# Performance work log

Measured on AMD Instinct MI355X. Metric: run time of the kernel, lower is better.

## Reference

```python
import jax, jax.numpy as jnp
import numpy as np

INV_SQRT2 = 0.7071067811865476
SCALES = 3


def dwt_analysis(x, dec_lo, dec_hi, scales):
    """Multi-level 1D DWT along last axis (pywt/ptwt convention).
    x: [B, D]. dec_lo/dec_hi are cross-correlation filters (torch conv1d
    semantics, i.e. the flipped pywt decomposition filters as stored by the
    repo). Returns [cA_s | cD_s | ... | cD_1] truncated to the last D columns
    (identity for Haar on power-of-two D)."""
    flen = dec_lo.shape[0]
    pad = (2 * flen - 3) // 2  # ptwt zero-pad; 0 for Haar (flen=2)
    filt = jnp.stack([dec_lo, dec_hi])[:, None, :]  # [2, 1, flen]
    lo = x[:, None, :]  # [B, 1, D]
    highs = []
    for _ in range(scales):
        out = jax.lax.conv_general_dilated(
            lo, filt, window_strides=(2,), padding=[(pad, pad)],
            dimension_numbers=('NCH', 'OIH', 'NCH'))  # [B, 2, D/2]
        lo = out[:, 0:1, :]
        highs.append(out[:, 1, :])
    coeffs = jnp.concatenate([lo[:, 0, :]] + highs[::-1], axis=-1)
    return coeffs[:, -x.shape[-1]:]


def setup_inputs() -> dict:
    key = jax.random.key(0)
    k1, k2, k3, k4, k5 = jax.random.split(key, 5)
    B, D = 4096, 4096
    x = jax.random.normal(k1, (B, D), jnp.float32)
    diag_s = jax.random.normal(k2, (D,), jnp.float32)
    diag_g = jax.random.normal(k3, (D,), jnp.float32)
    diag_b = jax.random.normal(k4, (D,), jnp.float32)
    perm = jax.random.permutation(k5, jnp.arange(D))  # random column permutation
    # Haar analysis filters in cross-correlation (torch conv1d) orientation
    dec_lo = jnp.array([INV_SQRT2, INV_SQRT2], jnp.float32)
    dec_hi = jnp.array([INV_SQRT2, -INV_SQRT2], jnp.float32)
    return {"x": x, "diag_s": diag_s, "diag_g": diag_g, "diag_b": diag_b,
            "dec_lo": dec_lo, "dec_hi": dec_hi, "perm": perm, "scales": SCALES}


def reference(x, diag_s, diag_g, diag_b, dec_lo, dec_hi, perm, scales):
    # mul_b: x @ diag(b) == columnwise scale (same math, no O(d^2) matmul)
    h = x * diag_b
    h = dwt_analysis(h, dec_lo, dec_hi, scales)
    # mul_p: x @ P for a permutation matrix == column gather
    h = jnp.take(h, perm, axis=1)
    h = h * diag_g  # mul_g
    h = dwt_analysis(h, dec_lo, dec_hi, scales)
    return h * diag_s  # mul_s
```

## Files before the change

kernel.cpp:

```cpp
#include <hip/hip_runtime.h>


#define D   4096
#define NT  256
#define R   4

#define C_INV_SQRT2 0.70710678118654752440f

typedef float vf2 __attribute__((ext_vector_type(2)));
typedef float vf4 __attribute__((ext_vector_type(4)));

static __device__ __forceinline__ int swz(int i) {
    return i ^ ((i >> 5) & 31);
}

static __device__ __forceinline__ void dwt3_reg(const float v[16],
                                                float a3[2], float d3[2],
                                                float d2[4], float d1[8]) {
    float a1[8];
    #pragma unroll
    for (int j = 0; j < 8; ++j) {
        a1[j] = (v[2 * j] + v[2 * j + 1]) * C_INV_SQRT2;
        d1[j] = (v[2 * j] - v[2 * j + 1]) * C_INV_SQRT2;
    }
    float a2[4];
    #pragma unroll
    for (int j = 0; j < 4; ++j) {
        a2[j] = (a1[2 * j] + a1[2 * j + 1]) * C_INV_SQRT2;
        d2[j] = (a1[2 * j] - a1[2 * j + 1]) * C_INV_SQRT2;
    }
    #pragma unroll
    for (int j = 0; j < 2; ++j) {
        a3[j] = (a2[2 * j] + a2[2 * j + 1]) * C_INV_SQRT2;
        d3[j] = (a2[2 * j] - a2[2 * j + 1]) * C_INV_SQRT2;
    }
}

__global__ __launch_bounds__(NT) void wavelet_rows_kernel(
    const float* __restrict__ x,
    const float* __restrict__ diag_s,
    const float* __restrict__ diag_g,
    const float* __restrict__ diag_b,
    const int*   __restrict__ perm,
    float*       __restrict__ out)
{
    __shared__ float buf[2][D];

    const int t = threadIdx.x;
    const size_t row0 = (size_t)blockIdx.x * R;

    float db[16], dg[16];
    int   pidx[16];
    {
        const vf4* b4 = (const vf4*)diag_b;
        const vf4* g4 = (const vf4*)diag_g;
        const int4* p4 = (const int4*)perm;
        #pragma unroll
        for (int k = 0; k < 4; ++k) {
            vf4 bv = b4[4 * t + k];
            db[4 * k + 0] = bv.x; db[4 * k + 1] = bv.y;
            db[4 * k + 2] = bv.z; db[4 * k + 3] = bv.w;
            vf4 gv = g4[4 * t + k];
            dg[4 * k + 0] = gv.x; dg[4 * k + 1] = gv.y;
            dg[4 * k + 2] = gv.z; dg[4 * k + 3] = gv.w;
            int4 pv = p4[4 * t + k];
            pidx[4 * k + 0] = pv.x; pidx[4 * k + 1] = pv.y;
            pidx[4 * k + 2] = pv.z; pidx[4 * k + 3] = pv.w;
        }
    }
    vf2 sA, sD3;
    vf4 sD2, sD1a, sD1b;
    {
        const vf2* s2 = (const vf2*)diag_s;
        const vf4* s4 = (const vf4*)diag_s;
        sA   = s2[t];
        sD3  = s2[256 + t];
        sD2  = s4[256 + t];
        sD1a = s4[512 + 2 * t];
        sD1b = s4[512 + 2 * t + 1];
    }

    for (int r = 0; r < R; ++r) {
        float* b = buf[r & 1];
        const vf4* x4 = (const vf4*)(x + (row0 + r) * (size_t)D);

        float v[16];
        #pragma unroll
        for (int k = 0; k < 4; ++k) {
            vf4 xv = x4[4 * t + k];
            v[4 * k + 0] = xv.x * db[4 * k + 0];
            v[4 * k + 1] = xv.y * db[4 * k + 1];
            v[4 * k + 2] = xv.z * db[4 * k + 2];
            v[4 * k + 3] = xv.w * db[4 * k + 3];
        }

        float a3[2], d3[2], d2[4], d1[8];
        dwt3_reg(v, a3, d3, d2, d1);

        #pragma unroll
        for (int j = 0; j < 2; ++j) b[swz(2 * t + j)]        = a3[j];
        #pragma unroll
        for (int j = 0; j < 2; ++j) b[swz(512 + 2 * t + j)]  = d3[j];
        #pragma unroll
        for (int j = 0; j < 4; ++j) b[swz(1024 + 4 * t + j)] = d2[j];
        #pragma unroll
        for (int j = 0; j < 8; ++j) b[swz(2048 + 8 * t + j)] = d1[j];

        __syncthreads();

        float w[16];
        #pragma unroll
        for (int k = 0; k < 16; ++k) {
            w[k] = b[swz(pidx[k])] * dg[k];
        }

        float b3[2], e3[2], e2[4], e1[8];
        dwt3_reg(w, b3, e3, e2, e1);

        float* orow = out + (row0 + r) * (size_t)D;
        {
            vf2* o2 = (vf2*)orow;
            vf2 ov;
            ov.x = b3[0] * sA.x;  ov.y = b3[1] * sA.y;
            __builtin_nontemporal_store(ov, &o2[t]);
            ov.x = e3[0] * sD3.x; ov.y = e3[1] * sD3.y;
            __builtin_nontemporal_store(ov, &o2[256 + t]);

            vf4* o4 = (vf4*)orow;
            vf4 o;
            o.x = e2[0] * sD2.x; o.y = e2[1] * sD2.y;
            o.z = e2[2] * sD2.z; o.w = e2[3] * sD2.w;
            __builtin_nontemporal_store(o, &o4[256 + t]);
            o.x = e1[0] * sD1a.x; o.y = e1[1] * sD1a.y;
            o.z = e1[2] * sD1a.z; o.w = e1[3] * sD1a.w;
            __builtin_nontemporal_store(o, &o4[512 + 2 * t]);
            o.x = e1[4] * sD1b.x; o.y = e1[5] * sD1b.y;
            o.z = e1[6] * sD1b.z; o.w = e1[7] * sD1b.w;
            __builtin_nontemporal_store(o, &o4[512 + 2 * t + 1]);
        }
    }
}

extern "C" void kernel_launch(void* const* d_in, const int* in_sizes, int n_in,
                              void* d_out, int out_size, void* d_ws, size_t ws_size,
                              hipStream_t stream) {
    const float* x      = (const float*)d_in[0];
    const float* diag_s = (const float*)d_in[1];
    const float* diag_g = (const float*)d_in[2];
    const float* diag_b = (const float*)d_in[3];
    const int* perm     = (const int*)d_in[6];
    float* out          = (float*)d_out;

    const int B = 4096 / R;
    wavelet_rows_kernel<<<B, NT, 0, stream>>>(x, diag_s, diag_g, diag_b, perm, out);
}
```

Before: 128.7 us.

## Prefetch next row into registers and use lightweight LDS-only barrier

Software-pipelines the row loop: the next row of x is loaded into registers before the current row's DWT and LDS exchange, so global-load latency overlaps with compute. The loop is fully unrolled and the __syncthreads is replaced with an LDS-only wait plus s_barrier, which does not wait on outstanding global loads. Launch bounds now request 4 blocks per CU. The cost is extra registers for the prefetched row, which may pressure occupancy.

After: 149.3 us. +16.0%, slower.

```diff
diff --git a/kernel.cpp b/kernel.cpp
--- a/kernel.cpp
+++ b/kernel.cpp
@@ -12,6 +12,13 @@
 
 static __device__ __forceinline__ int swz(int i) {
     return i ^ ((i >> 5) & 31);
+}
+
+static __device__ __forceinline__ void lds_barrier() {
+    __builtin_amdgcn_sched_barrier(0);
+    asm volatile("s_waitcnt lgkmcnt(0)" ::: "memory");
+    __builtin_amdgcn_s_barrier();
+    __builtin_amdgcn_sched_barrier(0);
 }
 
 static __device__ __forceinline__ void dwt3_reg(const float v[16],
@@ -36,7 +43,7 @@
     }
 }
 
-__global__ __launch_bounds__(NT) void wavelet_rows_kernel(
+__global__ __launch_bounds__(NT, 4) void wavelet_rows_kernel(
     const float* __restrict__ x,
     const float* __restrict__ diag_s,
     const float* __restrict__ diag_g,
@@ -80,18 +87,30 @@
         sD1b = s4[512 + 2 * t + 1];
     }
 
+    vf4 xv[4];
+    {
+        const vf4* x4 = (const vf4*)(x + row0 * (size_t)D);
+        #pragma unroll
+        for (int k = 0; k < 4; ++k) xv[k] = x4[4 * t + k];
+    }
+
+    #pragma unroll
     for (int r = 0; r < R; ++r) {
         float* b = buf[r & 1];
-        const vf4* x4 = (const vf4*)(x + (row0 + r) * (size_t)D);
 
         float v[16];
         #pragma unroll
         for (int k = 0; k < 4; ++k) {
-            vf4 xv = x4[4 * t + k];
-            v[4 * k + 0] = xv.x * db[4 * k + 0];
-            v[4 * k + 1] = xv.y * db[4 * k + 1];
-            v[4 * k + 2] = xv.z * db[4 * k + 2];
-            v[4 * k + 3] = xv.w * db[4 * k + 3];
+            v[4 * k + 0] = xv[k].x * db[4 * k + 0];
+            v[4 * k + 1] = xv[k].y * db[4 * k + 1];
+            v[4 * k + 2] = xv[k].z * db[4 * k + 2];
+            v[4 * k + 3] = xv[k].w * db[4 * k + 3];
+        }
+
+        if (r + 1 < R) {
+            const vf4* xn = (const vf4*)(x + (row0 + r + 1) * (size_t)D);
+            #pragma unroll
+            for (int k = 0; k < 4; ++k) xv[k] = xn[4 * t + k];
         }
 
         float a3[2], d3[2], d2[4], d1[8];
@@ -106,7 +125,7 @@
         #pragma unroll
         for (int j = 0; j < 8; ++j) b[swz(2048 + 8 * t + j)] = d1[j];
 
-        __syncthreads();
+        lds_barrier();
 
         float w[16];
         #pragma unroll
```
